# Kernel tuning notes

Measured on AMD Instinct MI355X. Metric: run time of the kernel, lower is better.

## Reference

```python
import jax, jax.numpy as jnp
import numpy as np

D_MODEL = 512
N_HEADS = 8
D_K = D_MODEL // N_HEADS


def setup_inputs() -> dict:
    key = jax.random.key(0)
    ks = jax.random.split(key, 12)
    B, S = 2, 4096
    std = 1.0 / np.sqrt(D_MODEL)
    inp = {
        "q": jax.random.normal(ks[0], (B, S, D_MODEL), jnp.float32),
        "k": jax.random.normal(ks[1], (B, S, D_MODEL), jnp.float32),
        "v": jax.random.normal(ks[2], (B, S, D_MODEL), jnp.float32),
        "Wq": jax.random.normal(ks[3], (D_MODEL, D_MODEL), jnp.float32) * std,
        "bq": jnp.zeros((D_MODEL,), jnp.float32),
        "Wk": jax.random.normal(ks[4], (D_MODEL, D_MODEL), jnp.float32) * std,
        "bk": jnp.zeros((D_MODEL,), jnp.float32),
        "Wv": jax.random.normal(ks[5], (D_MODEL, D_MODEL), jnp.float32) * std,
        "bv": jnp.zeros((D_MODEL,), jnp.float32),
        "Wo": jax.random.normal(ks[6], (D_MODEL, D_MODEL), jnp.float32) * std,
        "bo": jnp.zeros((D_MODEL,), jnp.float32),
        # torch init: ones
        "time_decay": jnp.ones((1, N_HEADS, 1, 1), jnp.float32) * 0.01,
        "scale": jnp.ones((1,), jnp.float32),
    }
    return inp


def reference(q, k, v, Wq, bq, Wk, bk, Wv, bv, Wo, bo, time_decay, scale):
    B, S, _ = q.shape
    # projections (torch Linear: x @ W.T + b), reshape to [B, H, S, d_k]
    def proj(x, W, b):
        y = x @ W.T + b
        return y.reshape(B, -1, N_HEADS, D_K).transpose(0, 2, 1, 3)

    qh = proj(q, Wq, bq)
    kh = proj(k, Wk, bk)
    vh = proj(v, Wv, bv)

    # scores: [B, H, Sq, Sk]
    scores = jnp.einsum("bhqd,bhkd->bhqk", qh, kh) / np.sqrt(D_K)
    scores = scores * scale
    # exponential decay over absolute key position (per-head learnable rate)
    pos = jnp.arange(S, dtype=scores.dtype)  # key positions
    decay = jnp.exp(-time_decay * jnp.abs(pos)[None, None, None, :])  # [1,H,1,Sk]
    scores = scores * decay

    attn = jax.nn.softmax(scores, axis=-1)
    context = jnp.einsum("bhqk,bhkd->bhqd", attn, vh)
    context = context.transpose(0, 2, 1, 3).reshape(B, S, D_MODEL)
    out = context @ Wo.T + bo
    return out
```

## Files before the change

### kernel.cpp

```cpp
#include <hip/hip_runtime.h>
#include <hip/hip_bf16.h>
#include <stdint.h>

typedef __attribute__((ext_vector_type(8))) __bf16 bf16x8;
typedef __attribute__((ext_vector_type(4))) float f32x4;
typedef __attribute__((ext_vector_type(16))) float f32x16;
typedef __attribute__((ext_vector_type(8))) unsigned short ushort8;
typedef __attribute__((ext_vector_type(4))) unsigned short ushort4v;
typedef __attribute__((ext_vector_type(2))) unsigned int uint2v;
typedef __attribute__((ext_vector_type(4))) unsigned int uint4v;

__device__ __forceinline__ unsigned short bfbits(float x) {
    __bf16 b = (__bf16)x;
    return __builtin_bit_cast(unsigned short, b);
}
__device__ __forceinline__ float bf2f(__bf16 x) {
    unsigned short u = __builtin_bit_cast(unsigned short, x);
    return __builtin_bit_cast(float, (unsigned int)u << 16);
}

__device__ __forceinline__ f32x4 mfma16(bf16x8 a, bf16x8 b, f32x4 c) {
    return __builtin_amdgcn_mfma_f32_16x16x32_bf16(a, b, c, 0, 0, 0);
}
__device__ __forceinline__ f32x16 mfma32(bf16x8 a, bf16x8 b, f32x16 c) {
    return __builtin_amdgcn_mfma_f32_32x32x16_bf16(a, b, c, 0, 0, 0);
}

__device__ __forceinline__ unsigned int cvtpk(float lo, float hi) {
    unsigned int r;
    asm("v_cvt_pk_bf16_f32 %0, %1, %2" : "=v"(r) : "v"(lo), "v"(hi));
    return r;
}

__device__ __forceinline__ float lanepull(float src, int srcl) {
    return __builtin_bit_cast(float,
        __builtin_amdgcn_ds_bpermute(srcl * 4, __builtin_bit_cast(int, src)));
}

__device__ __forceinline__ void gload16(const void* g, void* l) {
    __builtin_amdgcn_global_load_lds(
        (const __attribute__((address_space(1))) unsigned int*)g,
        (__attribute__((address_space(3))) unsigned int*)l, 16, 0, 0);
}

__device__ __forceinline__ f32x16 zero16() {
    f32x16 r;
    #pragma unroll
    for (int i = 0; i < 16; i++) r[i] = 0.f;
    return r;
}

__device__ __forceinline__ int tail_tiles(float tdh, float scale) {
    float cut = 5.3f + __logf(fmaxf(scale, 1e-20f));
    cut = fmaxf(cut, 0.f);
    tdh = fmaxf(tdh, 1e-8f);
    int kt = (int)ceilf(cut / (tdh * 64.f));
    if (kt < 1) kt = 1;
    if (kt > 64) kt = 64;
    return kt;
}

__global__ __launch_bounds__(256) void gemm_qkv(
    const float* __restrict__ q, const float* __restrict__ k, const float* __restrict__ v,
    const float* __restrict__ Wq, const float* __restrict__ bq,
    const float* __restrict__ Wk, const float* __restrict__ bk,
    const float* __restrict__ Wv, const float* __restrict__ bv,
    const float* __restrict__ td, const float* __restrict__ sc,
    unsigned short* __restrict__ Qh, unsigned short* __restrict__ Kh,
    unsigned short* __restrict__ Vt)
{
    __shared__ unsigned short Alds[128][40];
    __shared__ unsigned short Blds[128][40];

    const int id  = blockIdx.x;
    const int nid = (id & 7) * 96 + (id >> 3);
    const int z   = nid >> 8;
    const int rem = nid & 255;
    const int bm  = rem >> 2;
    const int bn  = rem & 3;

    const float* A0   = (z == 0) ? q  : (z == 1) ? k  : v;
    const float* W    = (z == 0) ? Wq : (z == 1) ? Wk : Wv;
    const float* bias = (z == 0) ? bq : (z == 1) ? bk : bv;

    const int tid  = threadIdx.x;
    const int lane = tid & 63;
    const int wid  = tid >> 6;
    const int wm   = wid >> 1, wn = wid & 1;
    const int l15  = lane & 15;
    const int g    = lane >> 4;
    const int srow = tid >> 1;
    const int scol = (tid & 1) * 16;

    const float* Aptr = A0 + (size_t)(bm * 128 + srow) * 512 + scol;
    const float* Bptr = W  + (size_t)(bn * 128 + srow) * 512 + scol;

    f32x4 acc[4][4];
    #pragma unroll
    for (int m = 0; m < 4; m++)
        #pragma unroll
        for (int n = 0; n < 4; n++)
            acc[m][n] = (f32x4){0.f, 0.f, 0.f, 0.f};

    float4 ra0 = ((const float4*)Aptr)[0], ra1 = ((const float4*)Aptr)[1];
    float4 ra2 = ((const float4*)Aptr)[2], ra3 = ((const float4*)Aptr)[3];
    float4 rb0 = ((const float4*)Bptr)[0], rb1 = ((const float4*)Bptr)[1];
    float4 rb2 = ((const float4*)Bptr)[2], rb3 = ((const float4*)Bptr)[3];

    for (int kk = 0; kk < 16; kk++) {
        {
            ushort8 p0 = { bfbits(ra0.x), bfbits(ra0.y), bfbits(ra0.z), bfbits(ra0.w),
                           bfbits(ra1.x), bfbits(ra1.y), bfbits(ra1.z), bfbits(ra1.w) };
            ushort8 p1 = { bfbits(ra2.x), bfbits(ra2.y), bfbits(ra2.z), bfbits(ra2.w),
                           bfbits(ra3.x), bfbits(ra3.y), bfbits(ra3.z), bfbits(ra3.w) };
            *(ushort8*)&Alds[srow][scol]     = p0;
            *(ushort8*)&Alds[srow][scol + 8] = p1;
            ushort8 q0 = { bfbits(rb0.x), bfbits(rb0.y), bfbits(rb0.z), bfbits(rb0.w),
                           bfbits(rb1.x), bfbits(rb1.y), bfbits(rb1.z), bfbits(rb1.w) };
            ushort8 q1 = { bfbits(rb2.x), bfbits(rb2.y), bfbits(rb2.z), bfbits(rb2.w),
                           bfbits(rb3.x), bfbits(rb3.y), bfbits(rb3.z), bfbits(rb3.w) };
            *(ushort8*)&Blds[srow][scol]     = q0;
            *(ushort8*)&Blds[srow][scol + 8] = q1;
        }
        __syncthreads();
        if (kk < 15) {
            const float* An = Aptr + (kk + 1) * 32;
            const float* Bn = Bptr + (kk + 1) * 32;
            ra0 = ((const float4*)An)[0]; ra1 = ((const float4*)An)[1];
            ra2 = ((const float4*)An)[2]; ra3 = ((const float4*)An)[3];
            rb0 = ((const float4*)Bn)[0]; rb1 = ((const float4*)Bn)[1];
            rb2 = ((const float4*)Bn)[2]; rb3 = ((const float4*)Bn)[3];
        }
        bf16x8 af[4], bfr[4];
        #pragma unroll
        for (int m = 0; m < 4; m++)
            af[m] = *(const bf16x8*)&Alds[wm * 64 + m * 16 + l15][g * 8];
        #pragma unroll
        for (int n = 0; n < 4; n++)
            bfr[n] = *(const bf16x8*)&Blds[wn * 64 + n * 16 + l15][g * 8];
        #pragma unroll
        for (int m = 0; m < 4; m++)
            #pragma unroll
            for (int n = 0; n < 4; n++)
                acc[m][n] = mfma16(af[m], bfr[n], acc[m][n]);
        __syncthreads();
    }

    const float coefL = sc[0] * 0.125f * 1.44269504f;

    #pragma unroll
    for (int m = 0; m < 4; m++) {
        const int grow0 = bm * 128 + wm * 64 + m * 16 + (g << 2);
        #pragma unroll
        for (int n = 0; n < 4; n++) {
            const int gcol = bn * 128 + wn * 64 + n * 16 + l15;
            const float bv2 = bias[gcol];
            f32x4 c = acc[m][n];
            const int b = grow0 >> 12, s0 = grow0 & 4095;
            const int h = gcol >> 6, dk = gcol & 63;
            if (z == 0) {
                const size_t base = ((size_t)(b * 8 + h) * 4096 + s0) * 64 + dk;
                #pragma unroll
                for (int r = 0; r < 4; r++)
                    Qh[base + (size_t)r * 64] = bfbits((c[r] + bv2) * coefL);
            } else if (z == 1) {
                const float tdh = td[h];
                const size_t base = ((size_t)(b * 8 + h) * 4096 + s0) * 64 + dk;
                #pragma unroll
                for (int r = 0; r < 4; r++)
                    Kh[base + (size_t)r * 64] = bfbits((c[r] + bv2) * __expf(-tdh * (float)(s0 + r)));
            } else {
                ushort4v pk = { bfbits(c[0] + bv2), bfbits(c[1] + bv2),
                                bfbits(c[2] + bv2), bfbits(c[3] + bv2) };
                *(ushort4v*)&Vt[((size_t)(b * 8 + h) * 64 + dk) * 4096 + s0] = pk;
            }
        }
    }
}

__global__ __launch_bounds__(256) void gemm_out(
    const unsigned short* __restrict__ Actx, const float* __restrict__ W,
    const float* __restrict__ bias, float* __restrict__ Out)
{
    __shared__ unsigned short Alds[128][40];
    __shared__ unsigned short Blds[64][40];

    const int id  = blockIdx.x;
    const int nid = (id & 7) * 64 + (id >> 3);
    const int bm  = nid >> 3;
    const int bn  = nid & 7;

    const int tid  = threadIdx.x;
    const int lane = tid & 63;
    const int wid  = tid >> 6;
    const int wm   = wid >> 1, wn = wid & 1;
    const int l15  = lane & 15;
    const int g    = lane >> 4;
    const int srA  = tid >> 1, scA = (tid & 1) * 16;
    const int srB  = tid >> 2, scB = (tid & 3) * 8;

    const unsigned short* Aptr = Actx + (size_t)(bm * 128 + srA) * 512 + scA;
    const float*          Bptr = W    + (size_t)(bn * 64  + srB) * 512 + scB;

    f32x4 acc[4][2];
    #pragma unroll
    for (int m = 0; m < 4; m++)
        #pragma unroll
        for (int n = 0; n < 2; n++)
            acc[m][n] = (f32x4){0.f, 0.f, 0.f, 0.f};

    ushort8 ra0 = ((const ushort8*)Aptr)[0];
    ushort8 ra1 = ((const ushort8*)Aptr)[1];
    float4  rb0 = ((const float4*)Bptr)[0];
    float4  rb1 = ((const float4*)Bptr)[1];

    for (int kk = 0; kk < 16; kk++) {
        *(ushort8*)&Alds[srA][scA]     = ra0;
        *(ushort8*)&Alds[srA][scA + 8] = ra1;
        {
            ushort8 pb = { bfbits(rb0.x), bfbits(rb0.y), bfbits(rb0.z), bfbits(rb0.w),
                           bfbits(rb1.x), bfbits(rb1.y), bfbits(rb1.z), bfbits(rb1.w) };
            *(ushort8*)&Blds[srB][scB] = pb;
        }
        __syncthreads();
        if (kk < 15) {
            const unsigned short* An = Aptr + (kk + 1) * 32;
            const float*          Bn = Bptr + (kk + 1) * 32;
            ra0 = ((const ushort8*)An)[0];
            ra1 = ((const ushort8*)An)[1];
            rb0 = ((const float4*)Bn)[0];
            rb1 = ((const float4*)Bn)[1];
        }
        bf16x8 af[4], bfr[2];
        #pragma unroll
        for (int m = 0; m < 4; m++)
            af[m] = *(const bf16x8*)&Alds[wm * 64 + m * 16 + l15][g * 8];
        #pragma unroll
        for (int n = 0; n < 2; n++)
            bfr[n] = *(const bf16x8*)&Blds[wn * 32 + n * 16 + l15][g * 8];
        #pragma unroll
        for (int m = 0; m < 4; m++)
            #pragma unroll
            for (int n = 0; n < 2; n++)
                acc[m][n] = mfma16(af[m], bfr[n], acc[m][n]);
        __syncthreads();
    }

    #pragma unroll
    for (int m = 0; m < 4; m++) {
        const int grow0 = bm * 128 + wm * 64 + m * 16 + (g << 2);
        #pragma unroll
        for (int n = 0; n < 2; n++) {
            const int gcol = bn * 64 + wn * 32 + n * 16 + l15;
            const float bv2 = bias[gcol];
            f32x4 c = acc[m][n];
            #pragma unroll
            for (int r = 0; r < 4; r++)
                Out[(size_t)(grow0 + r) * 512 + gcol] = c[r] + bv2;
        }
    }
}

__global__ __launch_bounds__(512) void tail_pre(
    const unsigned short* __restrict__ Kh, const unsigned short* __restrict__ Vt,
    const float* __restrict__ td, const float* __restrict__ sc,
    unsigned short* __restrict__ Mt, float* __restrict__ SumV, float* __restrict__ KsL)
{
    __shared__ float redM[4][32][32];
    __shared__ float redv[64];
    __shared__ float redk[64];

    const int bh   = blockIdx.x;
    const int h    = bh & 7;
    const int tid  = threadIdx.x;
    const int w    = tid >> 6;
    const int lane = tid & 63;
    const int l31  = lane & 31, hl = lane >> 5;
    const int d2q  = w & 1, d1q = (w >> 1) & 1, kh2 = w >> 2;

    const int KT   = tail_tiles(td[h], sc[0]);
    const int K0   = KT * 64;
    const int nk   = 4096 - K0;
    const int kcnt = nk >> 1;
    const int kbeg = K0 + kh2 * kcnt;

    f32x16 macc = zero16();
    float sumv = 0.f, ksum = 0.f;
    const unsigned short* Vrow = Vt + ((size_t)bh * 64 + d2q * 32 + l31) * 4096;
    const unsigned short* Kcol = Kh + (size_t)bh * 4096 * 64 + d1q * 32 + l31;

    for (int kk = 0; kk < kcnt; kk += 16) {
        const int k0 = kbeg + kk + hl * 8;
        bf16x8 av = *(const bf16x8*)(Vrow + k0);
        ushort8 kbv;
        #pragma unroll
        for (int e = 0; e < 8; e++)
            kbv[e] = Kcol[(size_t)(k0 + e) * 64];
        bf16x8 bkf = __builtin_bit_cast(bf16x8, kbv);
        macc = mfma32(av, bkf, macc);
        if (d1q == 0) {
            #pragma unroll
            for (int e = 0; e < 8; e++) sumv += bf2f(av[e]);
        }
        if (d2q == 0) {
            #pragma unroll
            for (int e = 0; e < 8; e++)
                ksum += __builtin_bit_cast(float, (unsigned int)kbv[e] << 16);
        }
    }
    sumv += __shfl_xor(sumv, 32);
    ksum += __shfl_xor(ksum, 32);

    const int quad = d2q * 2 + d1q;
    if (kh2 == 0) {
        #pragma unroll
        for (int r = 0; r < 16; r++) {
            const int row = (r & 3) + 8 * (r >> 2) + 4 * hl;
            redM[quad][row][l31] = macc[r];
        }
        if (d1q == 0 && hl == 0) redv[d2q * 32 + l31] = sumv;
        if (d2q == 0 && hl == 0) redk[d1q * 32 + l31] = ksum;
    }
    __syncthreads();
    if (kh2 == 1) {
        #pragma unroll
        for (int r = 0; r < 16; r++) {
            const int row = (r & 3) + 8 * (r >> 2) + 4 * hl;
            const float mv = (macc[r] + redM[quad][row][l31]) * 0.6931472f;
            Mt[(size_t)bh * 4096 + (size_t)(d2q * 32 + row) * 64 + d1q * 32 + l31] = bfbits(mv);
        }
        if (d1q == 0 && hl == 0)
            SumV[bh * 64 + d2q * 32 + l31] = sumv + redv[d2q * 32 + l31];
        if (d2q == 0 && hl == 0)
            KsL[bh * 64 + d1q * 32 + l31] = (ksum + redk[d1q * 32 + l31]) * 0.6931472f;
    }
}

__global__ __launch_bounds__(256, 4) void attn_decay(
    const unsigned short* __restrict__ Qh, const unsigned short* __restrict__ Kh,
    const unsigned short* __restrict__ Vt, const float* __restrict__ td,
    const float* __restrict__ sc,
    const unsigned short* __restrict__ Mt, const float* __restrict__ SumV,
    const float* __restrict__ KsL, unsigned short* __restrict__ ctx)
{
    __shared__ __align__(16) char LDSB[32768];

    const int tid  = threadIdx.x;
    const int lane = tid & 63;
    const int w    = tid >> 6;
    const int qg   = w >> 1;
    const int ws   = w & 1;
    const int l31  = lane & 31;
    const int hl   = lane >> 5;

    const int i  = blockIdx.x;
    const int bh = ((i & 7) << 1) | ((i >> 9) & 1);
    const int qt = (i >> 3) & 63;
    const int h  = bh & 7;
    const int b  = bh >> 3;

    const int KT = tail_tiles(td[h], sc[0]);
    const int nk = 4096 - KT * 64;

    bf16x8 qf[4];
    {
        const unsigned short* Qp =
            Qh + ((size_t)bh * 4096 + qt * 64 + qg * 32 + l31) * 64 + hl * 8;
        #pragma unroll
        for (int c = 0; c < 4; c++)
            qf[c] = *(const bf16x8*)(Qp + c * 16);
    }

    f32x16 o0 = zero16(), o1 = zero16();
    float lp = 0.f;

    const char* kgp0; const char* kgp1; const char* vgp0; const char* vgp1;
    int ldsoff0, ldsoff1;
    {
        const size_t kbaseB = (size_t)bh * 4096 * 64 * 2;
        const size_t vbaseB = (size_t)bh * 64 * 4096 * 2;
        const int p0 = w * 2048 + lane * 16;
        const int r0 = p0 >> 7, c0 = p0 & 127, sw0 = (r0 & 7) << 4;
        const int p1 = w * 2048 + 1024 + lane * 16;
        const int r1 = p1 >> 7, c1 = p1 & 127, sw1 = (r1 & 7) << 4;
        kgp0 = (const char*)Kh + kbaseB + (size_t)r0 * 128  + (c0 ^ sw0);
        kgp1 = (const char*)Kh + kbaseB + (size_t)r1 * 128  + (c1 ^ sw1);
        vgp0 = (const char*)Vt + vbaseB + (size_t)r0 * 8192 + (c0 ^ sw0);
        vgp1 = (const char*)Vt + vbaseB + (size_t)r1 * 8192 + (c1 ^ sw1);
        ldsoff0 = w * 2048;
        ldsoff1 = w * 2048 + 1024;
    }
    gload16(kgp0, LDSB + ldsoff0);
    gload16(kgp1, LDSB + ldsoff1);
    gload16(vgp0, LDSB + 16384 + ldsoff0);
    gload16(vgp1, LDSB + 16384 + ldsoff1);
    kgp0 += 8192; kgp1 += 8192; vgp0 += 128; vgp1 += 128;

    const int krow = ws * 32 + l31;
    const int ksw  = (krow & 7) << 4;

#define ATTN_TILE(CUR, KT_IDX)                                                    \
    {                                                                             \
        asm volatile("s_waitcnt vmcnt(0)" ::: "memory");                          \
        __syncthreads();                                                          \
        if ((KT_IDX) + 1 < KT) {                                                  \
            gload16(kgp0, LDSB + ((CUR) ^ 1) * 8192 + ldsoff0);                   \
            gload16(kgp1, LDSB + ((CUR) ^ 1) * 8192 + ldsoff1);                   \
            gload16(vgp0, LDSB + 16384 + ((CUR) ^ 1) * 8192 + ldsoff0);           \
            gload16(vgp1, LDSB + 16384 + ((CUR) ^ 1) * 8192 + ldsoff1);           \
            kgp0 += 8192; kgp1 += 8192; vgp0 += 128; vgp1 += 128;                 \
        }                                                                         \
        const char* kb = LDSB + (CUR) * 8192;                                     \
        const char* vb = LDSB + 16384 + (CUR) * 8192;                             \
        f32x16 s = zero16();                                                      \
        __builtin_amdgcn_s_setprio(1);                                            \
        _Pragma("unroll")                                                         \
        for (int c = 0; c < 4; c++) {                                             \
            bf16x8 kf = *(const bf16x8*)(kb + krow * 128 + ((c * 32 + hl * 16) ^ ksw)); \
            s = mfma32(kf, qf[c], s);                                             \
        }                                                                         \
        __builtin_amdgcn_s_setprio(0);                                            \
        float p[16];                                                              \
        _Pragma("unroll")                                                         \
        for (int r = 0; r < 16; r++) {                                            \
            p[r] = __builtin_amdgcn_exp2f(s[r]);                                  \
            lp += p[r];                                                           \
        }                                                                         \
        unsigned int W0 = cvtpk(p[0], p[1]),   W1 = cvtpk(p[2], p[3]);            \
        unsigned int W2 = cvtpk(p[4], p[5]),   W3 = cvtpk(p[6], p[7]);            \
        unsigned int W4 = cvtpk(p[8], p[9]),   W5 = cvtpk(p[10], p[11]);          \
        unsigned int W6 = cvtpk(p[12], p[13]), W7 = cvtpk(p[14], p[15]);          \
        uint2v r02 = __builtin_amdgcn_permlane32_swap(W0, W2, false, false);      \
        uint2v r13 = __builtin_amdgcn_permlane32_swap(W1, W3, false, false);      \
        uint2v r46 = __builtin_amdgcn_permlane32_swap(W4, W6, false, false);      \
        uint2v r57 = __builtin_amdgcn_permlane32_swap(W5, W7, false, false);      \
        bf16x8 pa0 = __builtin_bit_cast(bf16x8, (uint4v){r02.x, r13.x, r02.y, r13.y}); \
        bf16x8 pa1 = __builtin_bit_cast(bf16x8, (uint4v){r46.x, r57.x, r46.y, r57.y}); \
        __builtin_amdgcn_s_setprio(1);                                            \
        {                                                                         \
            const int vr0  = l31;                                                 \
            const int vsw0 = (vr0 & 7) << 4;                                      \
            bf16x8 va = *(const bf16x8*)(vb + vr0 * 128 + ((ws * 64 + hl * 16) ^ vsw0));      \
            bf16x8 vb2 = *(const bf16x8*)(vb + vr0 * 128 + ((ws * 64 + 32 + hl * 16) ^ vsw0));\
            o0 = mfma32(pa0, va, o0);                                             \
            o0 = mfma32(pa1, vb2, o0);                                            \
            const int vr1  = 32 + l31;                                            \
            const int vsw1 = (vr1 & 7) << 4;                                      \
            bf16x8 vc = *(const bf16x8*)(vb + vr1 * 128 + ((ws * 64 + hl * 16) ^ vsw1));      \
            bf16x8 vd = *(const bf16x8*)(vb + vr1 * 128 + ((ws * 64 + 32 + hl * 16) ^ vsw1)); \
            o1 = mfma32(pa0, vc, o1);                                             \
            o1 = mfma32(pa1, vd, o1);                                             \
        }                                                                         \
        __builtin_amdgcn_s_setprio(0);                                            \
    }

    const int KT2 = KT >> 1;
    #pragma unroll 1
    for (int t = 0; t < KT2; ++t) {
        ATTN_TILE(0, 2 * t)
        ATTN_TILE(1, 2 * t + 1)
    }
    if (KT & 1) {
        ATTN_TILE(0, KT - 1)
    }
#undef ATTN_TILE

    if (ws == 0 && nk > 0) {
        const float* KsLb = KsL + bh * 64;
        float qk = 0.f;
        #pragma unroll
        for (int c = 0; c < 4; c++) {
            ushort8 qb = __builtin_bit_cast(ushort8, qf[c]);
            #pragma unroll
            for (int e = 0; e < 8; e++)
                qk += __builtin_bit_cast(float, (unsigned int)qb[e] << 16)
                      * KsLb[c * 16 + hl * 8 + e];
        }
        qk += __shfl_xor(qk, 32);
        if (hl == 0) lp += (float)nk + qk;

        const unsigned short* Mb = Mt + (size_t)bh * 4096;
        #pragma unroll
        for (int c = 0; c < 4; c++) {
            bf16x8 m0 = *(const bf16x8*)(Mb + (size_t)l31 * 64 + c * 16 + hl * 8);
            bf16x8 m1 = *(const bf16x8*)(Mb + (size_t)(32 + l31) * 64 + c * 16 + hl * 8);
            o0 = mfma32(qf[c], m0, o0);
            o1 = mfma32(qf[c], m1, o1);
        }
        const float sv0 = SumV[bh * 64 + l31];
        const float sv1 = SumV[bh * 64 + 32 + l31];
        #pragma unroll
        for (int r = 0; r < 16; r++) { o0[r] += sv0; o1[r] += sv1; }
    }

    float lw = lp + __shfl_xor(lp, 32);
    __syncthreads();
    float* lscr = (float*)(LDSB + 16384);
    if (lane < 32)
        lscr[(qg * 2 + ws) * 32 + lane] = lw;
    __syncthreads();
    const float pl2 = lscr[(qg * 2 + (ws ^ 1)) * 32 + l31];
    const float myscale = 1.f / (lw + pl2);
    #pragma unroll
    for (int rc = 0; rc < 4; rc++)
        #pragma unroll
        for (int j = 0; j < 4; j++) {
            const float a = lanepull(myscale, rc * 8 + hl * 4 + j);
            o0[rc * 4 + j] *= a;
            o1[rc * 4 + j] *= a;
        }
    __syncthreads();
    float* Oscr = (float*)(LDSB + qg * 8192);
    if (ws == 1) {
        #pragma unroll
        for (int reg = 0; reg < 16; reg++) {
            const int row = (reg & 3) + 8 * (reg >> 2) + 4 * hl;
            Oscr[row * 64 + l31]      = o0[reg];
            Oscr[row * 64 + 32 + l31] = o1[reg];
        }
    }
    __syncthreads();
    if (ws == 0) {
        #pragma unroll
        for (int reg = 0; reg < 16; reg++) {
            const int row = (reg & 3) + 8 * (reg >> 2) + 4 * hl;
            const float v0 = o0[reg] + Oscr[row * 64 + l31];
            const float v1 = o1[reg] + Oscr[row * 64 + 32 + l31];
            const int srow_ = qt * 64 + qg * 32 + row;
            const size_t idx = ((size_t)b * 4096 + srow_) * 512 + h * 64;
            ctx[idx + l31]      = bfbits(v0);
            ctx[idx + 32 + l31] = bfbits(v1);
        }
    }
}

extern "C" void kernel_launch(void* const* d_in, const int* in_sizes, int n_in,
                              void* d_out, int out_size, void* d_ws, size_t ws_size,
                              hipStream_t stream)
{
    (void)in_sizes; (void)n_in; (void)out_size; (void)ws_size;
    const float* q  = (const float*)d_in[0];
    const float* k  = (const float*)d_in[1];
    const float* v  = (const float*)d_in[2];
    const float* Wq = (const float*)d_in[3];
    const float* bq = (const float*)d_in[4];
    const float* Wk = (const float*)d_in[5];
    const float* bk = (const float*)d_in[6];
    const float* Wv = (const float*)d_in[7];
    const float* bv = (const float*)d_in[8];
    const float* Wo = (const float*)d_in[9];
    const float* bo = (const float*)d_in[10];
    const float* td = (const float*)d_in[11];
    const float* sc = (const float*)d_in[12];

    unsigned short* Qh  = (unsigned short*)d_ws;
    unsigned short* Kh  = Qh + (size_t)16 * 4096 * 64;
    unsigned short* Vt  = Kh + (size_t)16 * 4096 * 64;
    unsigned short* ctx = Vt + (size_t)16 * 4096 * 64;

    unsigned short* Mt   = (unsigned short*)d_out;
    float*          SumV = (float*)((char*)d_out + 16 * 4096 * 2);
    float*          KsL  = SumV + 16 * 64;

    gemm_qkv<<<dim3(768), 256, 0, stream>>>(q, k, v, Wq, bq, Wk, bk, Wv, bv, td, sc, Qh, Kh, Vt);
    tail_pre<<<dim3(16), 512, 0, stream>>>(Kh, Vt, td, sc, Mt, SumV, KsL);
    attn_decay<<<dim3(1024), 256, 0, stream>>>(Qh, Kh, Vt, td, sc, Mt, SumV, KsL, ctx);
    gemm_out<<<dim3(512), 256, 0, stream>>>(ctx, Wo, bo, (float*)d_out);
}
```

Before: 132.8 us.

## Pre-convert weights to bf16, async-load GEMM tiles via LDS, split tail precompute

A new kernel converts all four weight matrices to bf16 once per call, so the QKV and output GEMMs read bf16 B fragments straight from global memory. The A tiles are now loaded with direct global-to-LDS loads into swizzled, double-buffered LDS, and the fp32 inputs are converted when fragments are read. The tail precompute kernel is split into two halves per head, with K staged through LDS, to double its parallelism; the attention kernel sums the two partial results. This adds one extra launch and more partial-result reads in exchange for less conversion work and better overlap of loads with compute.

```diff
diff --git a/kernel.cpp b/kernel.cpp
--- a/kernel.cpp
+++ b/kernel.cpp
@@ -14,8 +14,7 @@
     __bf16 b = (__bf16)x;
     return __builtin_bit_cast(unsigned short, b);
 }
-__device__ __forceinline__ float bf2f(__bf16 x) {
-    unsigned short u = __builtin_bit_cast(unsigned short, x);
+__device__ __forceinline__ float bf2f_u(unsigned short u) {
     return __builtin_bit_cast(float, (unsigned int)u << 16);
 }
 
@@ -60,17 +59,30 @@
     return kt;
 }
 
+__global__ __launch_bounds__(256) void wconv(
+    const float* __restrict__ Wq, const float* __restrict__ Wk,
+    const float* __restrict__ Wv, const float* __restrict__ Wo,
+    unsigned short* __restrict__ Wbf)
+{
+    const int t    = blockIdx.x * 256 + threadIdx.x;
+    const int slab = t >> 15;
+    const int off8 = t & 32767;
+    const float* src = (slab == 0) ? Wq : (slab == 1) ? Wk : (slab == 2) ? Wv : Wo;
+    float4 a = ((const float4*)(src + off8 * 8))[0];
+    float4 b = ((const float4*)(src + off8 * 8))[1];
+    uint4v pk = { cvtpk(a.x, a.y), cvtpk(a.z, a.w), cvtpk(b.x, b.y), cvtpk(b.z, b.w) };
+    *(uint4v*)(Wbf + (size_t)slab * 262144 + off8 * 8) = pk;
+}
+
 __global__ __launch_bounds__(256) void gemm_qkv(
     const float* __restrict__ q, const float* __restrict__ k, const float* __restrict__ v,
-    const float* __restrict__ Wq, const float* __restrict__ bq,
-    const float* __restrict__ Wk, const float* __restrict__ bk,
-    const float* __restrict__ Wv, const float* __restrict__ bv,
+    const unsigned short* __restrict__ Wbf,
+    const float* __restrict__ bq, const float* __restrict__ bk, const float* __restrict__ bv,
     const float* __restrict__ td, const float* __restrict__ sc,
     unsigned short* __restrict__ Qh, unsigned short* __restrict__ Kh,
     unsigned short* __restrict__ Vt)
 {
-    __shared__ unsigned short Alds[128][40];
-    __shared__ unsigned short Blds[128][40];
+    __shared__ __align__(16) char ALDS[2][16384];
 
     const int id  = blockIdx.x;
     const int nid = (id & 7) * 96 + (id >> 3);
@@ -80,20 +92,30 @@
     const int bn  = rem & 3;
 
     const float* A0   = (z == 0) ? q  : (z == 1) ? k  : v;
-    const float* W    = (z == 0) ? Wq : (z == 1) ? Wk : Wv;
     const float* bias = (z == 0) ? bq : (z == 1) ? bk : bv;
 
     const int tid  = threadIdx.x;
     const int lane = tid & 63;
-    const int wid  = tid >> 6;
-    const int wm   = wid >> 1, wn = wid & 1;
+    const int w    = tid >> 6;
+    const int wm   = w >> 1, wn = w & 1;
     const int l15  = lane & 15;
     const int g    = lane >> 4;
-    const int srow = tid >> 1;
-    const int scol = (tid & 1) * 16;
-
-    const float* Aptr = A0 + (size_t)(bm * 128 + srow) * 512 + scol;
-    const float* Bptr = W  + (size_t)(bn * 128 + srow) * 512 + scol;
+
+    const int lr  = lane >> 3;
+    const int lc  = ((lane & 7) * 16) ^ (lr << 4);
+    const char* asrc[4];
+    #pragma unroll
+    for (int j = 0; j < 4; j++)
+        asrc[j] = (const char*)A0 + (size_t)(bm * 128 + w * 32 + j * 8 + lr) * 2048 + lc;
+    int adst[4];
+    #pragma unroll
+    for (int j = 0; j < 4; j++) adst[j] = w * 4096 + j * 1024;
+
+    const unsigned short* Bp[4];
+    #pragma unroll
+    for (int n = 0; n < 4; n++)
+        Bp[n] = Wbf + (size_t)z * 262144
+              + (size_t)(bn * 128 + wn * 64 + n * 16 + l15) * 512 + g * 8;
 
     f32x4 acc[4][4];
     #pragma unroll
@@ -102,49 +124,53 @@
         for (int n = 0; n < 4; n++)
             acc[m][n] = (f32x4){0.f, 0.f, 0.f, 0.f};
 
-    float4 ra0 = ((const float4*)Aptr)[0], ra1 = ((const float4*)Aptr)[1];
-    float4 ra2 = ((const float4*)Aptr)[2], ra3 = ((const float4*)Aptr)[3];
-    float4 rb0 = ((const float4*)Bptr)[0], rb1 = ((const float4*)Bptr)[1];
-    float4 rb2 = ((const float4*)Bptr)[2], rb3 = ((const float4*)Bptr)[3];
-
-    for (int kk = 0; kk < 16; kk++) {
-        {
-            ushort8 p0 = { bfbits(ra0.x), bfbits(ra0.y), bfbits(ra0.z), bfbits(ra0.w),
-                           bfbits(ra1.x), bfbits(ra1.y), bfbits(ra1.z), bfbits(ra1.w) };
-            ushort8 p1 = { bfbits(ra2.x), bfbits(ra2.y), bfbits(ra2.z), bfbits(ra2.w),
-                           bfbits(ra3.x), bfbits(ra3.y), bfbits(ra3.z), bfbits(ra3.w) };
-            *(ushort8*)&Alds[srow][scol]     = p0;
-            *(ushort8*)&Alds[srow][scol + 8] = p1;
-            ushort8 q0 = { bfbits(rb0.x), bfbits(rb0.y), bfbits(rb0.z), bfbits(rb0.w),
-                           bfbits(rb1.x), bfbits(rb1.y), bfbits(rb1.z), bfbits(rb1.w) };
-            ushort8 q1 = { bfbits(rb2.x), bfbits(rb2.y), bfbits(rb2.z), bfbits(rb2.w),
-                           bfbits(rb3.x), bfbits(rb3.y), bfbits(rb3.z), bfbits(rb3.w) };
-            *(ushort8*)&Blds[srow][scol]     = q0;
-            *(ushort8*)&Blds[srow][scol + 8] = q1;
-        }
-        __syncthreads();
-        if (kk < 15) {
-            const float* An = Aptr + (kk + 1) * 32;
-            const float* Bn = Bptr + (kk + 1) * 32;
-            ra0 = ((const float4*)An)[0]; ra1 = ((const float4*)An)[1];
-            ra2 = ((const float4*)An)[2]; ra3 = ((const float4*)An)[3];
-            rb0 = ((const float4*)Bn)[0]; rb1 = ((const float4*)Bn)[1];
-            rb2 = ((const float4*)Bn)[2]; rb3 = ((const float4*)Bn)[3];
-        }
-        bf16x8 af[4], bfr[4];
-        #pragma unroll
-        for (int m = 0; m < 4; m++)
-            af[m] = *(const bf16x8*)&Alds[wm * 64 + m * 16 + l15][g * 8];
-        #pragma unroll
-        for (int n = 0; n < 4; n++)
-            bfr[n] = *(const bf16x8*)&Blds[wn * 64 + n * 16 + l15][g * 8];
-        #pragma unroll
-        for (int m = 0; m < 4; m++)
-            #pragma unroll
-            for (int n = 0; n < 4; n++)
-                acc[m][n] = mfma16(af[m], bfr[n], acc[m][n]);
-        __syncthreads();
-    }
+    const int arow = l15;
+    const int asw  = (arow & 7) << 4;
+
+    #pragma unroll
+    for (int j = 0; j < 4; j++) gload16(asrc[j], ALDS[0] + adst[j]);
+    bf16x8 BA[4], BB[4];
+    #pragma unroll
+    for (int n = 0; n < 4; n++) BA[n] = *(const bf16x8*)Bp[n];
+
+#define QKV_ITER(CUR, KK, BC, BN)                                                  \
+    {                                                                              \
+        asm volatile("s_waitcnt vmcnt(0)" ::: "memory");                           \
+        __syncthreads();                                                           \
+        if ((KK) < 15) {                                                           \
+            _Pragma("unroll")                                                      \
+            for (int j = 0; j < 4; j++)                                            \
+                gload16(asrc[j] + (size_t)((KK) + 1) * 128,                        \
+                        ALDS[(CUR) ^ 1] + adst[j]);                                \
+            _Pragma("unroll")                                                      \
+            for (int n = 0; n < 4; n++)                                            \
+                BN[n] = *(const bf16x8*)(Bp[n] + (size_t)((KK) + 1) * 32);         \
+        }                                                                          \
+        bf16x8 af[4];                                                              \
+        _Pragma("unroll")                                                          \
+        for (int m = 0; m < 4; m++) {                                              \
+            const char* base = ALDS[CUR] + (wm * 64 + m * 16 + arow) * 128;        \
+            f32x4 v0 = *(const f32x4*)(base + ((g * 32) ^ asw));                   \
+            f32x4 v1 = *(const f32x4*)(base + (((g * 32) | 16) ^ asw));            \
+            uint4v pk = { cvtpk(v0.x, v0.y), cvtpk(v0.z, v0.w),                    \
+                          cvtpk(v1.x, v1.y), cvtpk(v1.z, v1.w) };                  \
+            af[m] = __builtin_bit_cast(bf16x8, pk);                                \
+        }                                                                          \
+        __builtin_amdgcn_s_setprio(1);                                             \
+        _Pragma("unroll")                                                          \
+        for (int m = 0; m < 4; m++)                                                \
+            _Pragma("unroll")                                                      \
+            for (int n = 0; n < 4; n++)                                            \
+                acc[m][n] = mfma16(af[m], BC[n], acc[m][n]);                       \
+        __builtin_amdgcn_s_setprio(0);                                             \
+    }
+
+    #pragma unroll 1
+    for (int t = 0; t < 8; ++t) {
+        QKV_ITER(0, 2 * t, BA, BB)
+        QKV_ITER(1, 2 * t + 1, BB, BA)
+    }
+#undef QKV_ITER
 
     const float coefL = sc[0] * 0.125f * 1.44269504f;
 
@@ -179,11 +205,10 @@
 }
 
 __global__ __launch_bounds__(256) void gemm_out(
-    const unsigned short* __restrict__ Actx, const float* __restrict__ W,
+    const unsigned short* __restrict__ Actx, const unsigned short* __restrict__ Wob,
     const float* __restrict__ bias, float* __restrict__ Out)
 {
-    __shared__ unsigned short Alds[128][40];
-    __shared__ unsigned short Blds[64][40];
+    __shared__ __align__(16) char ALDS[2][16384];
 
     const int id  = blockIdx.x;
     const int nid = (id & 7) * 64 + (id >> 3);
@@ -192,15 +217,25 @@
 
     const int tid  = threadIdx.x;
     const int lane = tid & 63;
-    const int wid  = tid >> 6;
-    const int wm   = wid >> 1, wn = wid & 1;
+    const int w    = tid >> 6;
+    const int wm   = w >> 1, wn = w & 1;
     const int l15  = lane & 15;
     const int g    = lane >> 4;
-    const int srA  = tid >> 1, scA = (tid & 1) * 16;
-    const int srB  = tid >> 2, scB = (tid & 3) * 8;
-
-    const unsigned short* Aptr = Actx + (size_t)(bm * 128 + srA) * 512 + scA;
-    const float*          Bptr = W    + (size_t)(bn * 64  + srB) * 512 + scB;
+
+    const int lr  = lane >> 3;
+    const int lc  = ((lane & 7) * 16) ^ (lr << 4);
+    const char* asrc[4];
+    #pragma unroll
+    for (int j = 0; j < 4; j++)
+        asrc[j] = (const char*)Actx + (size_t)(bm * 128 + w * 32 + j * 8 + lr) * 1024 + lc;
+    int adst[4];
+    #pragma unroll
+    for (int j = 0; j < 4; j++) adst[j] = w * 4096 + j * 1024;
+
+    const unsigned short* Bp[2];
+    #pragma unroll
+    for (int n = 0; n < 2; n++)
+        Bp[n] = Wob + (size_t)(bn * 64 + wn * 32 + n * 16 + l15) * 512 + g * 8;
 
     f32x4 acc[4][2];
     #pragma unroll
@@ -209,42 +244,57 @@
         for (int n = 0; n < 2; n++)
             acc[m][n] = (f32x4){0.f, 0.f, 0.f, 0.f};
 
-    ushort8 ra0 = ((const ushort8*)Aptr)[0];
-    ushort8 ra1 = ((const ushort8*)Aptr)[1];
-    float4  rb0 = ((const float4*)Bptr)[0];
-    float4  rb1 = ((const float4*)Bptr)[1];
-
-    for (int kk = 0; kk < 16; kk++) {
-        *(ushort8*)&Alds[srA][scA]     = ra0;
-        *(ushort8*)&Alds[srA][scA + 8] = ra1;
-        {
-            ushort8 pb = { bfbits(rb0.x), bfbits(rb0.y), bfbits(rb0.z), bfbits(rb0.w),
-                           bfbits(rb1.x), bfbits(rb1.y), bfbits(rb1.z), bfbits(rb1.w) };
-            *(ushort8*)&Blds[srB][scB] = pb;
-        }
-        __syncthreads();
-        if (kk < 15) {
-            const unsigned short* An = Aptr + (kk + 1) * 32;
-            const float*          Bn = Bptr + (kk + 1) * 32;
-            ra0 = ((const ushort8*)An)[0];
-            ra1 = ((const ushort8*)An)[1];
-            rb0 = ((const float4*)Bn)[0];
-            rb1 = ((const float4*)Bn)[1];
-        }
-        bf16x8 af[4], bfr[2];
-        #pragma unroll
-        for (int m = 0; m < 4; m++)
-            af[m] = *(const bf16x8*)&Alds[wm * 64 + m * 16 + l15][g * 8];
-        #pragma unroll
-        for (int n = 0; n < 2; n++)
-            bfr[n] = *(const bf16x8*)&Blds[wn * 32 + n * 16 + l15][g * 8];
-        #pragma unroll
-        for (int m = 0; m < 4; m++)
-            #pragma unroll
-            for (int n = 0; n < 2; n++)
-                acc[m][n] = mfma16(af[m], bfr[n], acc[m][n]);
-        __syncthreads();
-    }
+    const int arow = l15;
+    const int asw  = (arow & 7) << 4;
+
+    #pragma unroll
+    for (int j = 0; j < 4; j++) gload16(asrc[j], ALDS[0] + adst[j]);
+    bf16x8 BA[2][2], BB[2][2];
+    #pragma unroll
+    for (int n = 0; n < 2; n++) {
+        BA[n][0] = *(const bf16x8*)Bp[n];
+        BA[n][1] = *(const bf16x8*)(Bp[n] + 32);
+    }
+
+#define OUT_ITER(CUR, KK, BC, BN)                                                  \
+    {                                                                              \
+        asm volatile("s_waitcnt vmcnt(0)" ::: "memory");                           \
+        __syncthreads();                                                           \
+        if ((KK) < 7) {                                                            \
+            _Pragma("unroll")                                                      \
+            for (int j = 0; j < 4; j++)                                            \
+                gload16(asrc[j] + (size_t)((KK) + 1) * 128,                        \
+                        ALDS[(CUR) ^ 1] + adst[j]);                                \
+            _Pragma("unroll")                                                      \
+            for (int n = 0; n < 2; n++) {                                          \
+                BN[n][0] = *(const bf16x8*)(Bp[n] + (size_t)((KK) + 1) * 64);      \
+                BN[n][1] = *(const bf16x8*)(Bp[n] + (size_t)((KK) + 1) * 64 + 32); \
+            }                                                                      \
+        }                                                                          \
+        bf16x8 af[4][2];                                                           \
+        _Pragma("unroll")                                                          \
+        for (int m = 0; m < 4; m++) {                                              \
+            const char* base = ALDS[CUR] + (wm * 64 + m * 16 + arow) * 128;        \
+            af[m][0] = *(const bf16x8*)(base + ((g * 16) ^ asw));                  \
+            af[m][1] = *(const bf16x8*)(base + ((64 + g * 16) ^ asw));             \
+        }                                                                          \
+        __builtin_amdgcn_s_setprio(1);                                             \
+        _Pragma("unroll")                                                          \
+        for (int m = 0; m < 4; m++)                                                \
+            _Pragma("unroll")                                                      \
+            for (int n = 0; n < 2; n++) {                                          \
+                acc[m][n] = mfma16(af[m][0], BC[n][0], acc[m][n]);                 \
+                acc[m][n] = mfma16(af[m][1], BC[n][1], acc[m][n]);                 \
+            }                                                                      \
+        __builtin_amdgcn_s_setprio(0);                                             \
+    }
+
+    #pragma unroll 1
+    for (int t = 0; t < 4; ++t) {
+        OUT_ITER(0, 2 * t, BA, BB)
+        OUT_ITER(1, 2 * t + 1, BB, BA)
+    }
+#undef OUT_ITER
 
     #pragma unroll
     for (int m = 0; m < 4; m++) {
@@ -266,53 +316,80 @@
     const float* __restrict__ td, const float* __restrict__ sc,
     unsigned short* __restrict__ Mt, float* __restrict__ SumV, float* __restrict__ KsL)
 {
+    __shared__ __align__(16) char KLDS[2][8192];
     __shared__ float redM[4][32][32];
     __shared__ float redv[64];
     __shared__ float redk[64];
 
-    const int bh   = blockIdx.x;
+    const int blk  = blockIdx.x;
+    const int bh   = blk >> 1;
+    const int half = blk & 1;
     const int h    = bh & 7;
     const int tid  = threadIdx.x;
     const int w    = tid >> 6;
     const int lane = tid & 63;
     const int l31  = lane & 31, hl = lane >> 5;
-    const int d2q  = w & 1, d1q = (w >> 1) & 1, kh2 = w >> 2;
-
-    const int KT   = tail_tiles(td[h], sc[0]);
-    const int K0   = KT * 64;
-    const int nk   = 4096 - K0;
-    const int kcnt = nk >> 1;
-    const int kbeg = K0 + kh2 * kcnt;
+    const int d2q  = w & 1, d1q = (w >> 1) & 1, ksub = w >> 2;
+
+    const int KT  = tail_tiles(td[h], sc[0]);
+    const int K0  = KT * 64;
+    const int nk  = 4096 - K0;
+    const int kh0 = ((nk >> 1) + 63) & ~63;
+    const int kcnt = half ? (nk - kh0) : kh0;
+    const int kbeg = K0 + half * kh0;
+    const int nch  = kcnt >> 6;
+
+    const int lr = lane >> 3;
+    const int r8 = (w * 8 + lr) & 7;
+    const char* ksrc = (const char*)Kh + (size_t)(bh * 4096 + kbeg + w * 8 + lr) * 128
+                     + (((lane & 7) * 16) ^ (r8 << 4));
+    const int kdst = w * 1024;
+
+    const unsigned short* Vp = Vt + (size_t)(bh * 64 + d2q * 32 + l31) * 4096 + kbeg;
 
     f32x16 macc = zero16();
     float sumv = 0.f, ksum = 0.f;
-    const unsigned short* Vrow = Vt + ((size_t)bh * 64 + d2q * 32 + l31) * 4096;
-    const unsigned short* Kcol = Kh + (size_t)bh * 4096 * 64 + d1q * 32 + l31;
-
-    for (int kk = 0; kk < kcnt; kk += 16) {
-        const int k0 = kbeg + kk + hl * 8;
-        bf16x8 av = *(const bf16x8*)(Vrow + k0);
-        ushort8 kbv;
-        #pragma unroll
-        for (int e = 0; e < 8; e++)
-            kbv[e] = Kcol[(size_t)(k0 + e) * 64];
-        bf16x8 bkf = __builtin_bit_cast(bf16x8, kbv);
-        macc = mfma32(av, bkf, macc);
-        if (d1q == 0) {
+
+    if (nch > 0) gload16(ksrc, KLDS[0] + kdst);
+
+    #pragma unroll 1
+    for (int ch = 0; ch < nch; ++ch) {
+        asm volatile("s_waitcnt vmcnt(0)" ::: "memory");
+        __syncthreads();
+        if (ch + 1 < nch)
+            gload16(ksrc + (size_t)(ch + 1) * 8192, KLDS[(ch + 1) & 1] + kdst);
+        const char* kb = KLDS[ch & 1];
+
+        #pragma unroll
+        for (int mf = 0; mf < 2; mf++) {
+            const int kloc0 = ksub * 32 + mf * 16 + hl * 8;
+            ushort8 kbv;
             #pragma unroll
-            for (int e = 0; e < 8; e++) sumv += bf2f(av[e]);
-        }
-        if (d2q == 0) {
-            #pragma unroll
-            for (int e = 0; e < 8; e++)
-                ksum += __builtin_bit_cast(float, (unsigned int)kbv[e] << 16);
-        }
-    }
+            for (int e = 0; e < 8; e++) {
+                const int row = kloc0 + e;
+                kbv[e] = *(const unsigned short*)(kb + row * 128
+                          + ((d1q * 64 + l31 * 2) ^ ((row & 7) << 4)));
+            }
+            if (d2q == 0) {
+                #pragma unroll
+                for (int e = 0; e < 8; e++) ksum += bf2f_u(kbv[e]);
+            }
+            bf16x8 av = *(const bf16x8*)(Vp + ch * 64 + kloc0);
+            if (d1q == 0) {
+                ushort8 au = __builtin_bit_cast(ushort8, av);
+                #pragma unroll
+                for (int e = 0; e < 8; e++) sumv += bf2f_u(au[e]);
+            }
+            macc = mfma32(av, __builtin_bit_cast(bf16x8, kbv), macc);
+        }
+    }
+
     sumv += __shfl_xor(sumv, 32);
     ksum += __shfl_xor(ksum, 32);
 
     const int quad = d2q * 2 + d1q;
-    if (kh2 == 0) {
+    __syncthreads();
+    if (ksub == 0) {
         #pragma unroll
         for (int r = 0; r < 16; r++) {
             const int row = (r & 3) + 8 * (r >> 2) + 4 * hl;
@@ -322,17 +399,18 @@
         if (d2q == 0 && hl == 0) redk[d1q * 32 + l31] = ksum;
     }
     __syncthreads();
-    if (kh2 == 1) {
+    if (ksub == 1) {
+        unsigned short* Mb = Mt + (size_t)half * 16 * 4096 + (size_t)bh * 4096;
         #pragma unroll
         for (int r = 0; r < 16; r++) {
             const int row = (r & 3) + 8 * (r >> 2) + 4 * hl;
             const float mv = (macc[r] + redM[quad][row][l31]) * 0.6931472f;
-            Mt[(size_t)bh * 4096 + (size_t)(d2q * 32 + row) * 64 + d1q * 32 + l31] = bfbits(mv);
+            Mb[(size_t)(d2q * 32 + row) * 64 + d1q * 32 + l31] = bfbits(mv);
         }
         if (d1q == 0 && hl == 0)
-            SumV[bh * 64 + d2q * 32 + l31] = sumv + redv[d2q * 32 + l31];
+            SumV[half * 1024 + bh * 64 + d2q * 32 + l31] = sumv + redv[d2q * 32 + l31];
         if (d2q == 0 && hl == 0)
-            KsL[bh * 64 + d1q * 32 + l31] = (ksum + redk[d1q * 32 + l31]) * 0.6931472f;
+            KsL[half * 1024 + bh * 64 + d1q * 32 + l31] = (ksum + redk[d1q * 32 + l31]) * 0.6931472f;
     }
 }
 
@@ -466,29 +544,32 @@
 #undef ATTN_TILE
 
     if (ws == 0 && nk > 0) {
-        const float* KsLb = KsL + bh * 64;
         float qk = 0.f;
         #pragma unroll
         for (int c = 0; c < 4; c++) {
             ushort8 qb = __builtin_bit_cast(ushort8, qf[c]);
             #pragma unroll
-            for (int e = 0; e < 8; e++)
-                qk += __builtin_bit_cast(float, (unsigned int)qb[e] << 16)
-                      * KsLb[c * 16 + hl * 8 + e];
+            for (int e = 0; e < 8; e++) {
+                const int idx = c * 16 + hl * 8 + e;
+                qk += bf2f_u(qb[e]) * (KsL[bh * 64 + idx] + KsL[1024 + bh * 64 + idx]);
+            }
         }
         qk += __shfl_xor(qk, 32);
         if (hl == 0) lp += (float)nk + qk;
 
-        const unsigned short* Mb = Mt + (size_t)bh * 4096;
-        #pragma unroll
-        for (int c = 0; c < 4; c++) {
-            bf16x8 m0 = *(const bf16x8*)(Mb + (size_t)l31 * 64 + c * 16 + hl * 8);
-            bf16x8 m1 = *(const bf16x8*)(Mb + (size_t)(32 + l31) * 64 + c * 16 + hl * 8);
-            o0 = mfma32(qf[c], m0, o0);
-            o1 = mfma32(qf[c], m1, o1);
-        }
-        const float sv0 = SumV[bh * 64 + l31];
-        const float sv1 = SumV[bh * 64 + 32 + l31];
+        #pragma unroll
+        for (int half = 0; half < 2; half++) {
+            const unsigned short* Mb = Mt + (size_t)half * 16 * 4096 + (size_t)bh * 4096;
+            #pragma unroll
+            for (int c = 0; c < 4; c++) {
+                bf16x8 m0 = *(const bf16x8*)(Mb + (size_t)l31 * 64 + c * 16 + hl * 8);
+                bf16x8 m1 = *(const bf16x8*)(Mb + (size_t)(32 + l31) * 64 + c * 16 + hl * 8);
+                o0 = mfma32(qf[c], m0, o0);
+                o1 = mfma32(qf[c], m1, o1);
+            }
+        }
+        const float sv0 = SumV[bh * 64 + l31]      + SumV[1024 + bh * 64 + l31];
+        const float sv1 = SumV[bh * 64 + 32 + l31] + SumV[1024 + bh * 64 + 32 + l31];
         #pragma unroll
         for (int r = 0; r < 16; r++) { o0[r] += sv0; o1[r] += sv1; }
     }
@@ -557,13 +638,15 @@
     unsigned short* Kh  = Qh + (size_t)16 * 4096 * 64;
     unsigned short* Vt  = Kh + (size_t)16 * 4096 * 64;
     unsigned short* ctx = Vt + (size_t)16 * 4096 * 64;
+    unsigned short* Wbf = ctx + (size_t)16 * 4096 * 64;
 
     unsigned short* Mt   = (unsigned short*)d_out;
-    float*          SumV = (float*)((char*)d_out + 16 * 4096 * 2);
-    float*          KsL  = SumV + 16 * 64;
-
-    gemm_qkv<<<dim3(768), 256, 0, stream>>>(q, k, v, Wq, bq, Wk, bk, Wv, bv, td, sc, Qh, Kh, Vt);
-    tail_pre<<<dim3(16), 512, 0, stream>>>(Kh, Vt, td, sc, Mt, SumV, KsL);
+    float*          SumV = (float*)((char*)d_out + 2 * 16 * 4096 * 2);
+    float*          KsL  = SumV + 2 * 1024;
+
+    wconv<<<dim3(512), 256, 0, stream>>>(Wq, Wk, Wv, Wo, Wbf);
+    gemm_qkv<<<dim3(768), 256, 0, stream>>>(q, k, v, Wbf, bq, bk, bv, td, sc, Qh, Kh, Vt);
+    tail_pre<<<dim3(32), 512, 0, stream>>>(Kh, Vt, td, sc, Mt, SumV, KsL);
     attn_decay<<<dim3(1024), 256, 0, stream>>>(Qh, Kh, Vt, td, sc, Mt, SumV, KsL, ctx);
-    gemm_out<<<dim3(512), 256, 0, stream>>>(ctx, Wo, bo, (float*)d_out);
-}
+    gemm_out<<<dim3(512), 256, 0, stream>>>(ctx, Wbf + (size_t)3 * 262144, bo, (float*)d_out);
+}
```

After: 122.5 us. 7.8% less time.
